# Performance work log

Hardware: AMD Instinct MI355X
Metric: run time of the kernel (lower is better)

The kernel has to match this reference:

```python
import jax, jax.numpy as jnp
import numpy as np

B, ND, NK = 4096, 32, 64        # batch, num_drones, num_docks
FD, FK = 16, 16                  # nfeat_drone, nfeat_dock
NHID, H = 128, 4                 # hidden dim, attention heads
ALPHA = 0.2                      # leaky relu slope
NEG = -9e15                      # masking constant from torch code


def setup_inputs() -> dict:
    key = jax.random.key(0)
    ks = jax.random.split(key, 13)
    s = 0.1
    obs = jax.random.normal(ks[0], (B, ND * FD + NK * FK + ND * NK), jnp.float32)
    return {
        "obs": obs,
        # DroneDockGAT params (per-head projections + additive attention vectors)
        "W_drone": jax.random.normal(ks[1], (H, FD, NHID), jnp.float32) * s,
        "W_dock": jax.random.normal(ks[2], (H, FK, NHID), jnp.float32) * s,
        "a_src": jax.random.normal(ks[3], (H, NHID), jnp.float32) * s,
        "a_dst": jax.random.normal(ks[4], (H, NHID), jnp.float32) * s,
        # critic: Linear(nhid*num_drones,64) -> ReLU -> Linear(64,1)
        "Wc1": jax.random.normal(ks[5], (NHID * ND, 64), jnp.float32) * s,
        "bc1": jnp.zeros((64,), jnp.float32),
        "Wc2": jax.random.normal(ks[6], (64, 1), jnp.float32) * s,
        "bc2": jnp.zeros((1,), jnp.float32),
        # actor heads
        "Wad": jax.random.normal(ks[7], (NHID, NHID), jnp.float32) * s,
        "bad": jnp.zeros((NHID,), jnp.float32),
        "Wak": jax.random.normal(ks[8], (NHID, NHID), jnp.float32) * s,
        "bak": jnp.zeros((NHID,), jnp.float32),
    }


def reference(obs, W_drone, W_dock, a_src, a_dst, Wc1, bc1, Wc2, bc2, Wad, bad, Wak, bak):
    sd, sk = ND * FD, NK * FK
    drone = obs[:, :sd].reshape(B, ND, FD)
    dock = obs[:, sd:sd + sk].reshape(B, NK, FK)
    adj = obs[:, sd + sk:].reshape(B, ND, NK)

    # per-head projections: [B, H, ND, NHID] / [B, H, NK, NHID]
    Whd = jnp.einsum('bnf,hfk->bhnk', drone, W_drone)
    Whk = jnp.einsum('bmf,hfk->bhmk', dock, W_dock)

    # additive GAT attention scores e[b,h,n,m]
    e = jax.nn.leaky_relu(
        jnp.einsum('bhnk,hk->bhn', Whd, a_src)[:, :, :, None]
        + jnp.einsum('bhmk,hk->bhm', Whk, a_dst)[:, :, None, :],
        ALPHA,
    )
    e = jnp.where(adj[:, None, :, :] > 0, e, NEG)
    attn = jax.nn.softmax(e, axis=-1)

    # head-averaged outputs with ELU
    h_drone = jax.nn.elu(jnp.einsum('bhnm,bhmk->bnk', attn, Whk) / H)  # [B, ND, NHID]
    h_dock = jax.nn.elu(Whk.mean(axis=1))                               # [B, NK, NHID]

    # critic
    values = jax.nn.relu(h_drone.reshape(B, -1) @ Wc1 + bc1) @ Wc2 + bc2  # [B, 1]

    # actor: masked drone-dock score matrix
    q = h_drone @ Wad + bad
    k = h_dock @ Wak + bak
    scores = jnp.einsum('bnk,bmk->bnm', q, k)
    logits = jnp.where(adj > 0, scores, NEG)  # [B, ND, NK]
    return values, logits
```

## Files before the change

### kernel.cpp

```cpp
#include <hip/hip_runtime.h>
#include <math.h>

#define OBSD 3584
#define NEGC -9e15f

typedef short short8 __attribute__((ext_vector_type(8)));
typedef float float4v __attribute__((ext_vector_type(4)));

#define WS_MT_S   0
#define WS_U_F    8192
#define WS_W_F    8320
#define WS_C0_F   8448
#define WS_AW_F   8452
#define WS_WDMT_S 17160
#define WS_WFT_S  19208
#define WS_WC1H_S 32768
#define WS_WC1L_S 294912
#define WS_NEED_BYTES 1114112ull

__device__ __forceinline__ float elu_f(float x) {
    return x > 0.f ? x : (__expf(x) - 1.f);
}
__device__ __forceinline__ short f2bf(float f) {
    union { float f; unsigned u; } v; v.f = f;
    unsigned u = v.u;
    unsigned r = (u + 0x7fffu + ((u >> 16) & 1u)) >> 16;
    return (short)r;
}
__device__ __forceinline__ float b2f(short s) {
    union { unsigned u; float f; } v; v.u = ((unsigned)(unsigned short)s) << 16;
    return v.f;
}
__device__ __forceinline__ unsigned pk2(float a, float b) {
    return (unsigned)(unsigned short)f2bf(a) | ((unsigned)(unsigned short)f2bf(b) << 16);
}

__global__ __launch_bounds__(256) void setup_fold(
    const float* __restrict__ W_drone, const float* __restrict__ W_dock,
    const float* __restrict__ a_src, const float* __restrict__ a_dst,
    const float* __restrict__ Wad, const float* __restrict__ Wak,
    const float* __restrict__ bad, const float* __restrict__ bak,
    float* __restrict__ wsf, short* __restrict__ wss)
{
    const int t = threadIdx.x, bi = blockIdx.x;
    if (bi < 16) {
        __shared__ float sa[32 * 132];
        __shared__ float sb[32 * 132];
        const int r0 = (bi >> 2) * 32, i0 = (bi & 3) * 32;
        #pragma unroll
        for (int qq = 0; qq < 4; ++qq) {
            int e = (t + 256 * qq) * 4;
            int r = e >> 7, cc = e & 127;
            *(float4*)&sa[r * 132 + cc] = *(const float4*)&Wad[(r0 + r) * 128 + cc];
            *(float4*)&sb[r * 132 + cc] = *(const float4*)&Wak[(i0 + r) * 128 + cc];
        }
        __syncthreads();
        int rr = (t >> 4) * 2, ii = (t & 15) * 2;
        float a00 = 0.f, a01 = 0.f, a10 = 0.f, a11 = 0.f;
        for (int c = 0; c < 128; ++c) {
            float x0 = sa[rr * 132 + c], x1 = sa[(rr + 1) * 132 + c];
            float y0 = sb[ii * 132 + c], y1 = sb[(ii + 1) * 132 + c];
            a00 += x0 * y0; a01 += x0 * y1; a10 += x1 * y0; a11 += x1 * y1;
        }
        wss[WS_MT_S + (i0 + ii) * 128 + (r0 + rr)]         = f2bf(a00);
        wss[WS_MT_S + (i0 + ii + 1) * 128 + (r0 + rr)]     = f2bf(a01);
        wss[WS_MT_S + (i0 + ii) * 128 + (r0 + rr + 1)]     = f2bf(a10);
        wss[WS_MT_S + (i0 + ii + 1) * 128 + (r0 + rr + 1)] = f2bf(a11);
    } else if (bi == 16) {
        if (t < 128) {
            float acc = 0.f;
            for (int c = 0; c < 128; ++c) acc += Wad[t * 128 + c] * bak[c];
            wsf[WS_U_F + t] = acc;
        } else {
            int j = t - 128;
            float acc = 0.f;
            for (int c = 0; c < 128; ++c) acc += Wak[j * 128 + c] * bad[c];
            wsf[WS_W_F + j] = acc;
        }
        if (t == 0) {
            float acc = 0.f;
            for (int c = 0; c < 128; ++c) acc += bad[c] * bak[c];
            wsf[WS_C0_F] = acc;
        }
    } else {
        if (t < 64) {
            int h = t >> 4, f = t & 15;
            const float* wrow = W_drone + h * 2048 + f * 128;
            const float* arow = a_src + h * 128;
            float acc = 0.f;
            for (int k = 0; k < 128; ++k) acc += wrow[k] * arow[k];
            wsf[WS_AW_F + t] = acc;
        } else if (t < 128) {
            int tt = t - 64;
            int h = tt >> 4, f = tt & 15;
            const float* wrow = W_dock + h * 2048 + f * 128;
            const float* arow = a_dst + h * 128;
            float acc = 0.f;
            for (int k = 0; k < 128; ++k) acc += wrow[k] * arow[k];
            wsf[WS_AW_F + 64 + tt] = acc;
        }
        for (int idx = t; idx < 2048; idx += 256) {
            int k2 = idx >> 4, f = idx & 15;
            float v = 0.25f * (W_dock[f * 128 + k2] + W_dock[2048 + f * 128 + k2]
                             + W_dock[4096 + f * 128 + k2] + W_dock[6144 + f * 128 + k2]);
            wss[WS_WDMT_S + k2 * 16 + f] = f2bf(v);
        }
        for (int idx = t; idx < 8192; idx += 256) {
            int k2 = idx >> 6, f64 = idx & 63;
            float v = W_dock[(f64 >> 4) * 2048 + (f64 & 15) * 128 + k2];
            wss[WS_WFT_S + k2 * 64 + f64] = f2bf(v);
        }
    }
}

__global__ __launch_bounds__(256) void setup_wc1(
    const float* __restrict__ Wc1,
    short* __restrict__ wc1h, short* __restrict__ wc1l)
{
    const int col = blockIdx.x;
    for (int k = threadIdx.x; k < 4096; k += 256) {
        float v = Wc1[(size_t)k * 64 + col];
        short hi = f2bf(v);
        float lo = v - b2f(hi);
        wc1h[col * 4096 + k] = hi;
        wc1l[col * 4096 + k] = f2bf(lo);
    }
}

__global__ __launch_bounds__(256, 2) void k1_attn_hd(
    const float* __restrict__ obs,
    const float* __restrict__ wsf, const short* __restrict__ wss,
    short* __restrict__ hdg)
{
    __shared__ __align__(16) char sm[57856];
    short* sD   = (short*)(sm + 0);
    short* sK   = (short*)(sm + 1024);
    short* sAdj = (short*)(sm + 3072);
    float* sAw  = (float*)(sm + 7680);
    float* sSrc = (float*)(sm + 8192);
    float* sDst = (float*)(sm + 8704);
    short* sAt  = (short*)(sm + 9728);
    short* sT   = (short*)(sm + 28160);
    short* sHd  = (short*)(sm + 32768);
    short* sWf  = (short*)(sm + 41472);

    const int t = threadIdx.x;
    const int b = blockIdx.x;
    const float* obsrow = obs + (size_t)b * OBSD;
    const int L = t & 63, c = L & 15, q = L >> 4, w = t >> 6;

    #pragma unroll
    for (int i = 0; i < 4; ++i) {
        int q4 = t + 256 * i;
        if (q4 < 896) {
            float4 v = ((const float4*)obsrow)[q4];
            int e0 = q4 * 4;
            if (e0 < 512) {
                int n = e0 >> 4, f0 = e0 & 15;
                sD[(f0 + 0) * 32 + n] = f2bf(v.x);
                sD[(f0 + 1) * 32 + n] = f2bf(v.y);
                sD[(f0 + 2) * 32 + n] = f2bf(v.z);
                sD[(f0 + 3) * 32 + n] = f2bf(v.w);
            } else if (e0 < 1536) {
                int e = e0 - 512;
                int m = e >> 4, f0 = e & 15;
                sK[(f0 + 0) * 64 + m] = f2bf(v.x);
                sK[(f0 + 1) * 64 + m] = f2bf(v.y);
                sK[(f0 + 2) * 64 + m] = f2bf(v.z);
                sK[(f0 + 3) * 64 + m] = f2bf(v.w);
            } else {
                int e = e0 - 1536;
                int n = e >> 6, m0 = e & 63;
                uint2 pkd = { pk2(v.x, v.y), pk2(v.z, v.w) };
                *(uint2*)&sAdj[n * 72 + m0] = pkd;
            }
        }
    }
    #pragma unroll
    for (int i = 0; i < 4; ++i)
        ((uint4*)sWf)[t + 256 * i] = ((const uint4*)(wss + WS_WFT_S))[t + 256 * i];
    if (t < 128) sAw[t] = wsf[WS_AW_F + t];
    __syncthreads();

    if (t < 128) {
        int h = t >> 5, n = t & 31;
        float acc = 0.f;
        #pragma unroll
        for (int f = 0; f < 16; ++f) acc += b2f(sD[f * 32 + n]) * sAw[h * 16 + f];
        sSrc[h * 32 + n] = acc;
    }
    {
        int h = t >> 6, m = t & 63;
        float acc = 0.f;
        #pragma unroll
        for (int f = 0; f < 16; ++f) acc += b2f(sK[f * 64 + m]) * sAw[64 + h * 16 + f];
        sDst[h * 64 + m] = acc;
    }
    __syncthreads();

    {
        int row = t >> 1, j = t & 1;
        int h = row >> 5, n = row & 31, m0 = j * 32;
        float sv = sSrc[h * 32 + n];
        float e32[32];
        float pmax = -INFINITY;
        #pragma unroll
        for (int mm = 0; mm < 32; ++mm) {
            int m = m0 + mm;
            float e = sv + sDst[h * 64 + m];
            e = e > 0.f ? e : 0.2f * e;
            e = (b2f(sAdj[n * 72 + m]) > 0.f) ? e : NEGC;
            e32[mm] = e;
            pmax = fmaxf(pmax, e);
        }
        pmax = fmaxf(pmax, __shfl_xor(pmax, 1, 2));
        float psum = 0.f;
        #pragma unroll
        for (int mm = 0; mm < 32; ++mm) { e32[mm] = __expf(e32[mm] - pmax); psum += e32[mm]; }
        psum += __shfl_xor(psum, 1, 2);
        float rinv = 1.f / psum;
        unsigned* ab = (unsigned*)sAt;
        int ub = (h * 2304 + n * 72 + m0) >> 1;
        #pragma unroll
        for (int mm = 0; mm < 32; mm += 2)
            ab[ub + (mm >> 1)] = pk2(e32[mm] * rinv, e32[mm + 1] * rinv);
    }
    __syncthreads();

    {
        int h = w;
        float4v accT[2] = { {0,0,0,0}, {0,0,0,0} };
        #pragma unroll
        for (int mt = 0; mt < 2; ++mt)
            #pragma unroll
            for (int kq = 0; kq < 2; ++kq) {
                short8 a = *(const short8*)&sAt[h * 2304 + (mt * 16 + c) * 72 + kq * 32 + q * 8];
                short8 bb = *(const short8*)&sK[c * 64 + kq * 32 + q * 8];
                accT[mt] = __builtin_amdgcn_mfma_f32_16x16x32_bf16(a, bb, accT[mt], 0, 0, 0);
            }
        #pragma unroll
        for (int mt = 0; mt < 2; ++mt)
            #pragma unroll
            for (int i = 0; i < 4; ++i)
                sT[(mt * 16 + q * 4 + i) * 72 + h * 16 + c] = f2bf(accT[mt][i]);
    }
    __syncthreads();

    {
        int mt = w & 1, ntb = (w >> 1) * 4;
        float4v acc[4] = { {0,0,0,0}, {0,0,0,0}, {0,0,0,0}, {0,0,0,0} };
        #pragma unroll
        for (int kq = 0; kq < 2; ++kq) {
            short8 a = *(const short8*)&sT[(mt * 16 + c) * 72 + kq * 32 + q * 8];
            #pragma unroll
            for (int p = 0; p < 4; ++p) {
                short8 bb = *(const short8*)&sWf[((ntb + p) * 16 + c) * 64 + kq * 32 + q * 8];
                acc[p] = __builtin_amdgcn_mfma_f32_16x16x32_bf16(a, bb, acc[p], 0, 0, 0);
            }
        }
        #pragma unroll
        for (int p = 0; p < 4; ++p)
            #pragma unroll
            for (int i = 0; i < 4; ++i) {
                float v = elu_f(acc[p][i] * 0.25f);
                sHd[(mt * 16 + q * 4 + i) * 136 + (ntb + p) * 16 + c] = f2bf(v);
            }
    }
    __syncthreads();

    {
        int n = t >> 3, k2 = (t & 7) * 16;
        uint4 x0 = *(const uint4*)&sHd[n * 136 + k2];
        uint4 x1 = *(const uint4*)&sHd[n * 136 + k2 + 8];
        uint4* dst = (uint4*)(hdg + (size_t)b * 4096 + n * 128 + k2);
        dst[0] = x0; dst[1] = x1;
    }
}

__global__ __launch_bounds__(256) void k2_critic(
    const short* __restrict__ hdg,
    const float* __restrict__ Wc1, const float* __restrict__ bc1,
    const float* __restrict__ Wc2, const float* __restrict__ bc2,
    float* __restrict__ out_values)
{
    __shared__ __align__(16) char sm[46592];
    short* As   = (short*)(sm + 0);
    float* Wst  = (float*)(sm + 9216);
    short* Bh   = (short*)(sm + 27648);
    short* Blo  = (short*)(sm + 36864);
    float* bc1L = (float*)(sm + 46080);
    float* wc2L = (float*)(sm + 46336);

    const int t = threadIdx.x;
    const int r0 = blockIdx.x * 64;
    const int L = t & 63, c = L & 15, q = L >> 4, w = t >> 6;

    if (t < 64) { bc1L[t] = bc1[t]; wc2L[t] = Wc2[t]; }

    float4v acc[4] = { {0,0,0,0}, {0,0,0,0}, {0,0,0,0}, {0,0,0,0} };

    for (int kc = 0; kc < 64; ++kc) {
        __syncthreads();
        {
            int r = t >> 2, kk0 = (t & 3) * 16;
            const uint4* src = (const uint4*)(hdg + (size_t)(r0 + r) * 4096 + kc * 64 + kk0);
            *(uint4*)&As[r * 72 + kk0]     = src[0];
            *(uint4*)&As[r * 72 + kk0 + 8] = src[1];
        }
        {
            int el = t >> 2, j0 = (t & 3) * 16;
            const float4* src = (const float4*)&Wc1[(size_t)(kc * 64 + el) * 64 + j0];
            #pragma unroll
            for (int u = 0; u < 4; ++u)
                *(float4*)&Wst[el * 72 + j0 + 4 * u] = src[u];
        }
        __syncthreads();
        {
            int j = t & 63, elb = (t >> 6) * 16;
            #pragma unroll
            for (int e = 0; e < 16; e += 2) {
                float v0 = Wst[(elb + e) * 72 + j];
                float v1 = Wst[(elb + e + 1) * 72 + j];
                short h0 = f2bf(v0), h1 = f2bf(v1);
                float l0 = v0 - b2f(h0), l1 = v1 - b2f(h1);
                *(unsigned*)&Bh[j * 72 + elb + e]  = (unsigned)(unsigned short)h0 | ((unsigned)(unsigned short)h1 << 16);
                *(unsigned*)&Blo[j * 72 + elb + e] = (unsigned)(unsigned short)f2bf(l0) | ((unsigned)(unsigned short)f2bf(l1) << 16);
            }
        }
        __syncthreads();
        #pragma unroll
        for (int kq = 0; kq < 2; ++kq) {
            short8 a = *(const short8*)&As[(w * 16 + c) * 72 + kq * 32 + q * 8];
            #pragma unroll
            for (int ct = 0; ct < 4; ++ct) {
                short8 bh = *(const short8*)&Bh[(ct * 16 + c) * 72 + kq * 32 + q * 8];
                short8 bl = *(const short8*)&Blo[(ct * 16 + c) * 72 + kq * 32 + q * 8];
                acc[ct] = __builtin_amdgcn_mfma_f32_16x16x32_bf16(a, bh, acc[ct], 0, 0, 0);
                acc[ct] = __builtin_amdgcn_mfma_f32_16x16x32_bf16(a, bl, acc[ct], 0, 0, 0);
            }
        }
    }
    float bc2v = bc2[0];
    #pragma unroll
    for (int i = 0; i < 4; ++i) {
        float sv = 0.f;
        #pragma unroll
        for (int ct = 0; ct < 4; ++ct) {
            float pre = acc[ct][i] + bc1L[ct * 16 + c];
            pre = fmaxf(pre, 0.f);
            sv += pre * wc2L[ct * 16 + c];
        }
        sv += __shfl_xor(sv, 1, 16);
        sv += __shfl_xor(sv, 2, 16);
        sv += __shfl_xor(sv, 4, 16);
        sv += __shfl_xor(sv, 8, 16);
        if (c == 0) out_values[r0 + w * 16 + q * 4 + i] = sv + bc2v;
    }
}

__global__ __launch_bounds__(256) void k2_critic2(
    const short* __restrict__ hdg,
    const short* __restrict__ wc1h, const short* __restrict__ wc1l,
    const float* __restrict__ bc1,
    const float* __restrict__ Wc2, const float* __restrict__ bc2,
    float* __restrict__ out_values)
{
    __shared__ __align__(16) char sm[39936];
    short* As   = (short*)(sm + 0);
    short* Bh   = (short*)(sm + 4352);
    short* Bl   = (short*)(sm + 21760);
    float* bc1L = (float*)(sm + 39168);
    float* wc2L = (float*)(sm + 39424);
    float* red  = (float*)(sm + 39680);

    const int t = threadIdx.x;
    const int r0 = blockIdx.x * 16;
    const int L = t & 63, c = L & 15, q = L >> 4, w = t >> 6;

    if (t < 64) { bc1L[t] = bc1[t]; wc2L[t] = Wc2[t]; }

    float4v acc = {0, 0, 0, 0};

    const int rA  = t >> 4,  kkA = (t & 15) * 8;
    const int colB = t >> 2, kbB = (t & 3) * 32;

    for (int it = 0; it < 32; ++it) {
        const int kc = it * 128;
        __syncthreads();
        *(uint4*)&As[rA * 136 + kkA] =
            *(const uint4*)(hdg + (size_t)(r0 + rA) * 4096 + kc + kkA);
        {
            const uint4* srcH = (const uint4*)(wc1h + (size_t)colB * 4096 + kc + kbB);
            const uint4* srcL = (const uint4*)(wc1l + (size_t)colB * 4096 + kc + kbB);
            #pragma unroll
            for (int u = 0; u < 4; ++u) {
                *(uint4*)&Bh[colB * 136 + kbB + 8 * u] = srcH[u];
                *(uint4*)&Bl[colB * 136 + kbB + 8 * u] = srcL[u];
            }
        }
        __syncthreads();
        #pragma unroll
        for (int kq = 0; kq < 4; ++kq) {
            short8 a  = *(const short8*)&As[c * 136 + kq * 32 + q * 8];
            short8 bh = *(const short8*)&Bh[(w * 16 + c) * 136 + kq * 32 + q * 8];
            short8 bl = *(const short8*)&Bl[(w * 16 + c) * 136 + kq * 32 + q * 8];
            acc = __builtin_amdgcn_mfma_f32_16x16x32_bf16(a, bh, acc, 0, 0, 0);
            acc = __builtin_amdgcn_mfma_f32_16x16x32_bf16(a, bl, acc, 0, 0, 0);
        }
    }
    #pragma unroll
    for (int i = 0; i < 4; ++i) {
        float pre = acc[i] + bc1L[w * 16 + c];
        pre = fmaxf(pre, 0.f);
        float sv = pre * wc2L[w * 16 + c];
        sv += __shfl_xor(sv, 1, 16);
        sv += __shfl_xor(sv, 2, 16);
        sv += __shfl_xor(sv, 4, 16);
        sv += __shfl_xor(sv, 8, 16);
        if (c == 0) red[w * 16 + q * 4 + i] = sv;
    }
    __syncthreads();
    if (t < 16) {
        float v = red[t] + red[16 + t] + red[32 + t] + red[48 + t] + bc2[0];
        out_values[r0 + t] = v;
    }
}

__global__ __launch_bounds__(256, 2) void k3_logits(
    const float* __restrict__ obs,
    const float* __restrict__ wsf, const short* __restrict__ wss,
    float* __restrict__ out_logits)
{
    __shared__ __align__(16) char sm[75648];
    short* dockRm = (short*)(sm + 0);
    short* adjBf  = (short*)(sm + 2048);
    short* hdS    = (short*)(sm + 6656);
    short* hkS    = (short*)(sm + 15360);
    short* wdmTS  = (short*)(sm + 32768);
    short* t2S    = (short*)(sm + 32768);
    float* suL    = (float*)(sm + 41472);
    float* swL    = (float*)(sm + 41600);
    float* uL     = (float*)(sm + 41856);
    float* wL     = (float*)(sm + 42368);
    short* MtS    = (short*)(sm + 42880);

    const int t = threadIdx.x;
    const int b = blockIdx.x;
    const float* obsrow = obs + (size_t)b * OBSD;
    short* hdg = (short*)out_logits;
    const int L = t & 63, c = L & 15, q = L >> 4, w = t >> 6;

    {
        int n = t >> 3, k2 = (t & 7) * 16;
        const uint4* src = (const uint4*)(hdg + (size_t)b * 4096 + n * 128 + k2);
        uint4 x0 = src[0], x1 = src[1];
        *(uint4*)&hdS[n * 136 + k2]     = x0;
        *(uint4*)&hdS[n * 136 + k2 + 8] = x1;
    }
    {
        float4 v = ((const float4*)obsrow)[128 + t];
        int m = t >> 2, f0 = (t & 3) * 4;
        uint2 pkd = { pk2(v.x, v.y), pk2(v.z, v.w) };
        *(uint2*)&dockRm[m * 16 + f0] = pkd;
    }
    #pragma unroll
    for (int i = 0; i < 2; ++i) {
        int q4 = 384 + t + 256 * i;
        if (q4 < 896) {
            float4 v = ((const float4*)obsrow)[q4];
            int e = q4 * 4 - 1536;
            int n = e >> 6, m0 = e & 63;
            uint2 pkd = { pk2(v.x, v.y), pk2(v.z, v.w) };
            *(uint2*)&adjBf[n * 72 + m0] = pkd;
        }
    }
    ((uint4*)wdmTS)[t] = ((const uint4*)(wss + WS_WDMT_S))[t];
    #pragma unroll
    for (int i = 0; i < 8; ++i)
        ((uint4*)MtS)[t + 256 * i] = ((const uint4*)(wss + WS_MT_S))[t + 256 * i];
    if (t < 128) uL[t] = wsf[WS_U_F + t];
    else wL[t - 128] = wsf[WS_W_F + (t - 128)];
    __syncthreads();

    {
        int mt = w;
        short8 a;
        if (q < 2) a = *(const short8*)&dockRm[(mt * 16 + c) * 16 + q * 8];
        else a = short8{0, 0, 0, 0, 0, 0, 0, 0};
        float swp[4] = {0.f, 0.f, 0.f, 0.f};
        #pragma unroll
        for (int nt = 0; nt < 8; ++nt) {
            short8 bb;
            if (q < 2) bb = *(const short8*)&wdmTS[(nt * 16 + c) * 16 + q * 8];
            else bb = short8{0, 0, 0, 0, 0, 0, 0, 0};
            float4v acc = {0, 0, 0, 0};
            acc = __builtin_amdgcn_mfma_f32_16x16x32_bf16(a, bb, acc, 0, 0, 0);
            float wv = wL[nt * 16 + c];
            #pragma unroll
            for (int i = 0; i < 4; ++i) {
                float ev = elu_f(acc[i]);
                hkS[(mt * 16 + q * 4 + i) * 136 + nt * 16 + c] = f2bf(ev);
                swp[i] += ev * wv;
            }
        }
        #pragma unroll
        for (int i = 0; i < 4; ++i) {
            float sv = swp[i];
            sv += __shfl_xor(sv, 1, 16);
            sv += __shfl_xor(sv, 2, 16);
            sv += __shfl_xor(sv, 4, 16);
            sv += __shfl_xor(sv, 8, 16);
            if (c == 0) swL[mt * 16 + q * 4 + i] = sv;
        }
    }
    {
        int n = t >> 3, p = t & 7;
        float a = 0.f;
        #pragma unroll
        for (int kk = 0; kk < 16; kk += 2) {
            unsigned uu = *(const unsigned*)&hdS[n * 136 + p * 16 + kk];
            a += b2f((short)(uu & 0xffff)) * uL[p * 16 + kk]
               + b2f((short)(uu >> 16))   * uL[p * 16 + kk + 1];
        }
        a += __shfl_xor(a, 1, 8);
        a += __shfl_xor(a, 2, 8);
        a += __shfl_xor(a, 4, 8);
        if (p == 0) suL[n] = a;
    }
    __syncthreads();

    {
        int mt = w & 1, ntb = (w >> 1) * 4;
        float4v acc[4] = { {0,0,0,0}, {0,0,0,0}, {0,0,0,0}, {0,0,0,0} };
        #pragma unroll
        for (int kq = 0; kq < 4; ++kq) {
            short8 a = *(const short8*)&hdS[(mt * 16 + c) * 136 + kq * 32 + q * 8];
            #pragma unroll
            for (int p = 0; p < 4; ++p) {
                short8 bb = *(const short8*)&MtS[((ntb + p) * 16 + c) * 128 + kq * 32 + q * 8];
                acc[p] = __builtin_amdgcn_mfma_f32_16x16x32_bf16(a, bb, acc[p], 0, 0, 0);
            }
        }
        __syncthreads();
        #pragma unroll
        for (int p = 0; p < 4; ++p)
            #pragma unroll
            for (int i = 0; i < 4; ++i)
                t2S[(mt * 16 + q * 4 + i) * 136 + (ntb + p) * 16 + c] = f2bf(acc[p][i]);
    }
    __syncthreads();

    {
        const float c0v = wsf[WS_C0_F];
        int ntd = w;
        float* lg = out_logits + (size_t)b * 2048;
        #pragma unroll
        for (int mt = 0; mt < 2; ++mt) {
            float4v acc = {0, 0, 0, 0};
            #pragma unroll
            for (int kq = 0; kq < 4; ++kq) {
                short8 a  = *(const short8*)&t2S[(mt * 16 + c) * 136 + kq * 32 + q * 8];
                short8 bb = *(const short8*)&hkS[(ntd * 16 + c) * 136 + kq * 32 + q * 8];
                acc = __builtin_amdgcn_mfma_f32_16x16x32_bf16(a, bb, acc, 0, 0, 0);
            }
            int col = ntd * 16 + c;
            float swv = swL[col];
            #pragma unroll
            for (int i = 0; i < 4; ++i) {
                int row = mt * 16 + q * 4 + i;
                float val = acc[i] + suL[row] + swv + c0v;
                bool keep = b2f(adjBf[row * 72 + col]) > 0.f;
                lg[row * 64 + col] = keep ? val : NEGC;
            }
        }
    }
}

extern "C" void kernel_launch(void* const* d_in, const int* in_sizes, int n_in,
                              void* d_out, int out_size, void* d_ws, size_t ws_size,
                              hipStream_t stream) {
    (void)in_sizes; (void)n_in; (void)out_size;
    const float* obs     = (const float*)d_in[0];
    const float* W_drone = (const float*)d_in[1];
    const float* W_dock  = (const float*)d_in[2];
    const float* a_src   = (const float*)d_in[3];
    const float* a_dst   = (const float*)d_in[4];
    const float* Wc1     = (const float*)d_in[5];
    const float* bc1     = (const float*)d_in[6];
    const float* Wc2     = (const float*)d_in[7];
    const float* bc2     = (const float*)d_in[8];
    const float* Wad     = (const float*)d_in[9];
    const float* bad     = (const float*)d_in[10];
    const float* Wak     = (const float*)d_in[11];
    const float* bak     = (const float*)d_in[12];
    float* out = (float*)d_out;
    float* wsf = (float*)d_ws;
    short* wss = (short*)d_ws;
    short* hdg = (short*)(out + 4096);

    const bool big_ws = (ws_size >= WS_NEED_BYTES);

    setup_fold<<<dim3(18), dim3(256), 0, stream>>>(
        W_drone, W_dock, a_src, a_dst, Wad, Wak, bad, bak, wsf, wss);
    if (big_ws)
        setup_wc1<<<dim3(64), dim3(256), 0, stream>>>(
            Wc1, wss + WS_WC1H_S, wss + WS_WC1L_S);

    k1_attn_hd<<<dim3(4096), dim3(256), 0, stream>>>(obs, wsf, wss, hdg);

    if (big_ws)
        k2_critic2<<<dim3(256), dim3(256), 0, stream>>>(
            hdg, wss + WS_WC1H_S, wss + WS_WC1L_S, bc1, Wc2, bc2, out);
    else
        k2_critic<<<dim3(64), dim3(256), 0, stream>>>(hdg, Wc1, bc1, Wc2, bc2, out);

    k3_logits<<<dim3(4096), dim3(256), 0, stream>>>(obs, wsf, wss, out + 4096);
}
```

Before: 263.3 us.

## Fuse attention and actor-logits kernels per batch row; coalesce Wc1 split setup

Adds a fused kernel that computes the attention/h_drone stage and then, reusing the already-loaded adjacency and h_drone in shared memory, computes the actor logits in the same block. h_drone is staged in workspace rather than the output buffer, and the critic then runs afterward. This removes the separate logits kernel's obs reload and launch, and the round trip of h_drone, at the cost of more LDS per block (74KB), which can reduce occupancy. The Wc1 hi/lo split setup is also rewritten to use a shared-memory transpose with vectorized stores. The fused path only runs when the workspace is large enough.

```diff
diff --git a/kernel.cpp b/kernel.cpp
--- a/kernel.cpp
+++ b/kernel.cpp
@@ -16,7 +16,9 @@
 #define WS_WFT_S  19208
 #define WS_WC1H_S 32768
 #define WS_WC1L_S 294912
-#define WS_NEED_BYTES 1114112ull
+#define WS_HD_S   557056
+#define WS_NEED_BYTES  1114112ull
+#define WS_NEED2_BYTES 34668544ull
 
 __device__ __forceinline__ float elu_f(float x) {
     return x > 0.f ? x : (__expf(x) - 1.f);
@@ -117,32 +119,59 @@
     const float* __restrict__ Wc1,
     short* __restrict__ wc1h, short* __restrict__ wc1l)
 {
-    const int col = blockIdx.x;
-    for (int k = threadIdx.x; k < 4096; k += 256) {
-        float v = Wc1[(size_t)k * 64 + col];
-        short hi = f2bf(v);
-        float lo = v - b2f(hi);
-        wc1h[col * 4096 + k] = hi;
-        wc1l[col * 4096 + k] = f2bf(lo);
-    }
-}
-
-__global__ __launch_bounds__(256, 2) void k1_attn_hd(
+    __shared__ float tile[64 * 68];
+    const int t = threadIdx.x;
+    const int k0 = blockIdx.x * 64;
+    {
+        int r = t >> 2, c0 = (t & 3) * 16;
+        const float4* src = (const float4*)&Wc1[(size_t)(k0 + r) * 64 + c0];
+        #pragma unroll
+        for (int u = 0; u < 4; ++u)
+            *(float4*)&tile[r * 68 + c0 + 4 * u] = src[u];
+    }
+    __syncthreads();
+    {
+        int col = t >> 2, kk0 = (t & 3) * 16;
+        short hi[16], lo[16];
+        #pragma unroll
+        for (int j = 0; j < 16; ++j) {
+            float v = tile[(kk0 + j) * 68 + col];
+            hi[j] = f2bf(v);
+            lo[j] = f2bf(v - b2f(hi[j]));
+        }
+        uint4* dh = (uint4*)(wc1h + (size_t)col * 4096 + k0 + kk0);
+        uint4* dl = (uint4*)(wc1l + (size_t)col * 4096 + k0 + kk0);
+        dh[0] = *(uint4*)&hi[0]; dh[1] = *(uint4*)&hi[8];
+        dl[0] = *(uint4*)&lo[0]; dl[1] = *(uint4*)&lo[8];
+    }
+}
+
+__global__ __launch_bounds__(256, 2) void k13_fused(
     const float* __restrict__ obs,
     const float* __restrict__ wsf, const short* __restrict__ wss,
-    short* __restrict__ hdg)
+    short* __restrict__ hdg,
+    float* __restrict__ out_logits)
 {
-    __shared__ __align__(16) char sm[57856];
-    short* sD   = (short*)(sm + 0);
-    short* sK   = (short*)(sm + 1024);
-    short* sAdj = (short*)(sm + 3072);
-    float* sAw  = (float*)(sm + 7680);
-    float* sSrc = (float*)(sm + 8192);
-    float* sDst = (float*)(sm + 8704);
-    short* sAt  = (short*)(sm + 9728);
-    short* sT   = (short*)(sm + 28160);
-    short* sHd  = (short*)(sm + 32768);
-    short* sWf  = (short*)(sm + 41472);
+    __shared__ __align__(16) char sm[74240];
+    short* sD     = (short*)(sm + 0);
+    short* sK     = (short*)(sm + 1024);
+    short* sAdj   = (short*)(sm + 3072);
+    float* sAw    = (float*)(sm + 7680);
+    float* sSrc   = (float*)(sm + 8192);
+    float* sDst   = (float*)(sm + 8704);
+    short* sAt    = (short*)(sm + 9728);
+    short* sT     = (short*)(sm + 28160);
+    short* sHd    = (short*)(sm + 32768);
+    short* sWf    = (short*)(sm + 41472);
+    short* dockRm = (short*)(sm + 0);
+    float* suL    = (float*)(sm + 8192);
+    float* swL    = (float*)(sm + 8320);
+    float* uL     = (float*)(sm + 8704);
+    float* wL     = (float*)(sm + 9216);
+    short* hkS    = (short*)(sm + 9728);
+    short* wdmTS  = (short*)(sm + 28160);
+    short* t2S    = (short*)(sm + 32768);
+    short* MtS    = (short*)(sm + 41472);
 
     const int t = threadIdx.x;
     const int b = blockIdx.x;
@@ -275,6 +304,262 @@
         uint4* dst = (uint4*)(hdg + (size_t)b * 4096 + n * 128 + k2);
         dst[0] = x0; dst[1] = x1;
     }
+    {
+        float4 v = ((const float4*)obsrow)[128 + t];
+        int m = t >> 2, f0 = (t & 3) * 4;
+        uint2 pkd = { pk2(v.x, v.y), pk2(v.z, v.w) };
+        *(uint2*)&dockRm[m * 16 + f0] = pkd;
+    }
+    ((uint4*)wdmTS)[t] = ((const uint4*)(wss + WS_WDMT_S))[t];
+    #pragma unroll
+    for (int i = 0; i < 8; ++i)
+        ((uint4*)MtS)[t + 256 * i] = ((const uint4*)(wss + WS_MT_S))[t + 256 * i];
+    if (t < 128) uL[t] = wsf[WS_U_F + t];
+    else wL[t - 128] = wsf[WS_W_F + (t - 128)];
+    __syncthreads();
+
+    {
+        int mt = w;
+        short8 a;
+        if (q < 2) a = *(const short8*)&dockRm[(mt * 16 + c) * 16 + q * 8];
+        else a = short8{0, 0, 0, 0, 0, 0, 0, 0};
+        float swp[4] = {0.f, 0.f, 0.f, 0.f};
+        #pragma unroll
+        for (int nt = 0; nt < 8; ++nt) {
+            short8 bb;
+            if (q < 2) bb = *(const short8*)&wdmTS[(nt * 16 + c) * 16 + q * 8];
+            else bb = short8{0, 0, 0, 0, 0, 0, 0, 0};
+            float4v acc = {0, 0, 0, 0};
+            acc = __builtin_amdgcn_mfma_f32_16x16x32_bf16(a, bb, acc, 0, 0, 0);
+            float wv = wL[nt * 16 + c];
+            #pragma unroll
+            for (int i = 0; i < 4; ++i) {
+                float ev = elu_f(acc[i]);
+                hkS[(mt * 16 + q * 4 + i) * 136 + nt * 16 + c] = f2bf(ev);
+                swp[i] += ev * wv;
+            }
+        }
+        #pragma unroll
+        for (int i = 0; i < 4; ++i) {
+            float sv = swp[i];
+            sv += __shfl_xor(sv, 1, 16);
+            sv += __shfl_xor(sv, 2, 16);
+            sv += __shfl_xor(sv, 4, 16);
+            sv += __shfl_xor(sv, 8, 16);
+            if (c == 0) swL[mt * 16 + q * 4 + i] = sv;
+        }
+    }
+    {
+        int n = t >> 3, p = t & 7;
+        float a = 0.f;
+        #pragma unroll
+        for (int kk = 0; kk < 16; kk += 2) {
+            unsigned uu = *(const unsigned*)&sHd[n * 136 + p * 16 + kk];
+            a += b2f((short)(uu & 0xffff)) * uL[p * 16 + kk]
+               + b2f((short)(uu >> 16))   * uL[p * 16 + kk + 1];
+        }
+        a += __shfl_xor(a, 1, 8);
+        a += __shfl_xor(a, 2, 8);
+        a += __shfl_xor(a, 4, 8);
+        if (p == 0) suL[n] = a;
+    }
+    __syncthreads();
+
+    {
+        int mt = w & 1, ntb = (w >> 1) * 4;
+        float4v acc[4] = { {0,0,0,0}, {0,0,0,0}, {0,0,0,0}, {0,0,0,0} };
+        #pragma unroll
+        for (int kq = 0; kq < 4; ++kq) {
+            short8 a = *(const short8*)&sHd[(mt * 16 + c) * 136 + kq * 32 + q * 8];
+            #pragma unroll
+            for (int p = 0; p < 4; ++p) {
+                short8 bb = *(const short8*)&MtS[((ntb + p) * 16 + c) * 128 + kq * 32 + q * 8];
+                acc[p] = __builtin_amdgcn_mfma_f32_16x16x32_bf16(a, bb, acc[p], 0, 0, 0);
+            }
+        }
+        __syncthreads();
+        #pragma unroll
+        for (int p = 0; p < 4; ++p)
+            #pragma unroll
+            for (int i = 0; i < 4; ++i)
+                t2S[(mt * 16 + q * 4 + i) * 136 + (ntb + p) * 16 + c] = f2bf(acc[p][i]);
+    }
+    __syncthreads();
+
+    {
+        const float c0v = wsf[WS_C0_F];
+        int ntd = w;
+        float* lg = out_logits + (size_t)b * 2048;
+        #pragma unroll
+        for (int mt = 0; mt < 2; ++mt) {
+            float4v acc = {0, 0, 0, 0};
+            #pragma unroll
+            for (int kq = 0; kq < 4; ++kq) {
+                short8 a  = *(const short8*)&t2S[(mt * 16 + c) * 136 + kq * 32 + q * 8];
+                short8 bb = *(const short8*)&hkS[(ntd * 16 + c) * 136 + kq * 32 + q * 8];
+                acc = __builtin_amdgcn_mfma_f32_16x16x32_bf16(a, bb, acc, 0, 0, 0);
+            }
+            int col = ntd * 16 + c;
+            float swv = swL[col];
+            #pragma unroll
+            for (int i = 0; i < 4; ++i) {
+                int row = mt * 16 + q * 4 + i;
+                float val = acc[i] + suL[row] + swv + c0v;
+                bool keep = b2f(sAdj[row * 72 + col]) > 0.f;
+                lg[row * 64 + col] = keep ? val : NEGC;
+            }
+        }
+    }
+}
+
+__global__ __launch_bounds__(256, 2) void k1_attn_hd(
+    const float* __restrict__ obs,
+    const float* __restrict__ wsf, const short* __restrict__ wss,
+    short* __restrict__ hdg)
+{
+    __shared__ __align__(16) char sm[57856];
+    short* sD   = (short*)(sm + 0);
+    short* sK   = (short*)(sm + 1024);
+    short* sAdj = (short*)(sm + 3072);
+    float* sAw  = (float*)(sm + 7680);
+    float* sSrc = (float*)(sm + 8192);
+    float* sDst = (float*)(sm + 8704);
+    short* sAt  = (short*)(sm + 9728);
+    short* sT   = (short*)(sm + 28160);
+    short* sHd  = (short*)(sm + 32768);
+    short* sWf  = (short*)(sm + 41472);
+
+    const int t = threadIdx.x;
+    const int b = blockIdx.x;
+    const float* obsrow = obs + (size_t)b * OBSD;
+    const int L = t & 63, c = L & 15, q = L >> 4, w = t >> 6;
+
+    #pragma unroll
+    for (int i = 0; i < 4; ++i) {
+        int q4 = t + 256 * i;
+        if (q4 < 896) {
+            float4 v = ((const float4*)obsrow)[q4];
+            int e0 = q4 * 4;
+            if (e0 < 512) {
+                int n = e0 >> 4, f0 = e0 & 15;
+                sD[(f0 + 0) * 32 + n] = f2bf(v.x);
+                sD[(f0 + 1) * 32 + n] = f2bf(v.y);
+                sD[(f0 + 2) * 32 + n] = f2bf(v.z);
+                sD[(f0 + 3) * 32 + n] = f2bf(v.w);
+            } else if (e0 < 1536) {
+                int e = e0 - 512;
+                int m = e >> 4, f0 = e & 15;
+                sK[(f0 + 0) * 64 + m] = f2bf(v.x);
+                sK[(f0 + 1) * 64 + m] = f2bf(v.y);
+                sK[(f0 + 2) * 64 + m] = f2bf(v.z);
+                sK[(f0 + 3) * 64 + m] = f2bf(v.w);
+            } else {
+                int e = e0 - 1536;
+                int n = e >> 6, m0 = e & 63;
+                uint2 pkd = { pk2(v.x, v.y), pk2(v.z, v.w) };
+                *(uint2*)&sAdj[n * 72 + m0] = pkd;
+            }
+        }
+    }
+    #pragma unroll
+    for (int i = 0; i < 4; ++i)
+        ((uint4*)sWf)[t + 256 * i] = ((const uint4*)(wss + WS_WFT_S))[t + 256 * i];
+    if (t < 128) sAw[t] = wsf[WS_AW_F + t];
+    __syncthreads();
+
+    if (t < 128) {
+        int h = t >> 5, n = t & 31;
+        float acc = 0.f;
+        #pragma unroll
+        for (int f = 0; f < 16; ++f) acc += b2f(sD[f * 32 + n]) * sAw[h * 16 + f];
+        sSrc[h * 32 + n] = acc;
+    }
+    {
+        int h = t >> 6, m = t & 63;
+        float acc = 0.f;
+        #pragma unroll
+        for (int f = 0; f < 16; ++f) acc += b2f(sK[f * 64 + m]) * sAw[64 + h * 16 + f];
+        sDst[h * 64 + m] = acc;
+    }
+    __syncthreads();
+
+    {
+        int row = t >> 1, j = t & 1;
+        int h = row >> 5, n = row & 31, m0 = j * 32;
+        float sv = sSrc[h * 32 + n];
+        float e32[32];
+        float pmax = -INFINITY;
+        #pragma unroll
+        for (int mm = 0; mm < 32; ++mm) {
+            int m = m0 + mm;
+            float e = sv + sDst[h * 64 + m];
+            e = e > 0.f ? e : 0.2f * e;
+            e = (b2f(sAdj[n * 72 + m]) > 0.f) ? e : NEGC;
+            e32[mm] = e;
+            pmax = fmaxf(pmax, e);
+        }
+        pmax = fmaxf(pmax, __shfl_xor(pmax, 1, 2));
+        float psum = 0.f;
+        #pragma unroll
+        for (int mm = 0; mm < 32; ++mm) { e32[mm] = __expf(e32[mm] - pmax); psum += e32[mm]; }
+        psum += __shfl_xor(psum, 1, 2);
+        float rinv = 1.f / psum;
+        unsigned* ab = (unsigned*)sAt;
+        int ub = (h * 2304 + n * 72 + m0) >> 1;
+        #pragma unroll
+        for (int mm = 0; mm < 32; mm += 2)
+            ab[ub + (mm >> 1)] = pk2(e32[mm] * rinv, e32[mm + 1] * rinv);
+    }
+    __syncthreads();
+
+    {
+        int h = w;
+        float4v accT[2] = { {0,0,0,0}, {0,0,0,0} };
+        #pragma unroll
+        for (int mt = 0; mt < 2; ++mt)
+            #pragma unroll
+            for (int kq = 0; kq < 2; ++kq) {
+                short8 a = *(const short8*)&sAt[h * 2304 + (mt * 16 + c) * 72 + kq * 32 + q * 8];
+                short8 bb = *(const short8*)&sK[c * 64 + kq * 32 + q * 8];
+                accT[mt] = __builtin_amdgcn_mfma_f32_16x16x32_bf16(a, bb, accT[mt], 0, 0, 0);
+            }
+        #pragma unroll
+        for (int mt = 0; mt < 2; ++mt)
+            #pragma unroll
+            for (int i = 0; i < 4; ++i)
+                sT[(mt * 16 + q * 4 + i) * 72 + h * 16 + c] = f2bf(accT[mt][i]);
+    }
+    __syncthreads();
+
+    {
+        int mt = w & 1, ntb = (w >> 1) * 4;
+        float4v acc[4] = { {0,0,0,0}, {0,0,0,0}, {0,0,0,0}, {0,0,0,0} };
+        #pragma unroll
+        for (int kq = 0; kq < 2; ++kq) {
+            short8 a = *(const short8*)&sT[(mt * 16 + c) * 72 + kq * 32 + q * 8];
+            #pragma unroll
+            for (int p = 0; p < 4; ++p) {
+                short8 bb = *(const short8*)&sWf[((ntb + p) * 16 + c) * 64 + kq * 32 + q * 8];
+                acc[p] = __builtin_amdgcn_mfma_f32_16x16x32_bf16(a, bb, acc[p], 0, 0, 0);
+            }
+        }
+        #pragma unroll
+        for (int p = 0; p < 4; ++p)
+            #pragma unroll
+            for (int i = 0; i < 4; ++i) {
+                float v = elu_f(acc[p][i] * 0.25f);
+                sHd[(mt * 16 + q * 4 + i) * 136 + (ntb + p) * 16 + c] = f2bf(v);
+            }
+    }
+    __syncthreads();
+
+    {
+        int n = t >> 3, k2 = (t & 7) * 16;
+        uint4 x0 = *(const uint4*)&sHd[n * 136 + k2];
+        uint4 x1 = *(const uint4*)&sHd[n * 136 + k2 + 8];
+        uint4* dst = (uint4*)(hdg + (size_t)b * 4096 + n * 128 + k2);
+        dst[0] = x0; dst[1] = x1;
+    }
 }
 
 __global__ __launch_bounds__(256) void k2_critic(
@@ -596,23 +881,30 @@
     float* out = (float*)d_out;
     float* wsf = (float*)d_ws;
     short* wss = (short*)d_ws;
-    short* hdg = (short*)(out + 4096);
-
-    const bool big_ws = (ws_size >= WS_NEED_BYTES);
+
+    const bool ws_wc1 = (ws_size >= WS_NEED_BYTES);
+    const bool ws_hd  = (ws_size >= WS_NEED2_BYTES);
 
     setup_fold<<<dim3(18), dim3(256), 0, stream>>>(
         W_drone, W_dock, a_src, a_dst, Wad, Wak, bad, bak, wsf, wss);
-    if (big_ws)
+    if (ws_wc1)
         setup_wc1<<<dim3(64), dim3(256), 0, stream>>>(
             Wc1, wss + WS_WC1H_S, wss + WS_WC1L_S);
 
-    k1_attn_hd<<<dim3(4096), dim3(256), 0, stream>>>(obs, wsf, wss, hdg);
-
-    if (big_ws)
+    if (ws_hd) {
+        short* hdw = wss + WS_HD_S;
+        k13_fused<<<dim3(4096), dim3(256), 0, stream>>>(
+            obs, wsf, wss, hdw, out + 4096);
         k2_critic2<<<dim3(256), dim3(256), 0, stream>>>(
-            hdg, wss + WS_WC1H_S, wss + WS_WC1L_S, bc1, Wc2, bc2, out);
-    else
-        k2_critic<<<dim3(64), dim3(256), 0, stream>>>(hdg, Wc1, bc1, Wc2, bc2, out);
-
-    k3_logits<<<dim3(4096), dim3(256), 0, stream>>>(obs, wsf, wss, out + 4096);
-}
+            hdw, wss + WS_WC1H_S, wss + WS_WC1L_S, bc1, Wc2, bc2, out);
+    } else {
+        short* hdg = (short*)(out + 4096);
+        k1_attn_hd<<<dim3(4096), dim3(256), 0, stream>>>(obs, wsf, wss, hdg);
+        if (ws_wc1)
+            k2_critic2<<<dim3(256), dim3(256), 0, stream>>>(
+                hdg, wss + WS_WC1H_S, wss + WS_WC1L_S, bc1, Wc2, bc2, out);
+        else
+            k2_critic<<<dim3(64), dim3(256), 0, stream>>>(hdg, Wc1, bc1, Wc2, bc2, out);
+        k3_logits<<<dim3(4096), dim3(256), 0, stream>>>(obs, wsf, wss, out + 4096);
+    }
+}
```

After: 248.1 us. 1.06x faster.
